# Optimization experiments

Measured on AMD Instinct MI355X. Metric: run time of the kernel, lower is better.

The kernel has to match this reference:

```python
import jax, jax.numpy as jnp
import numpy as np

N_NODES = 100000


def gcn_conv(x, edge_index, edge_weight, W, b, num_nodes):
    """PyG-style GCNConv: add self-loops, symmetric normalization, aggregate, linear."""
    src, dst = edge_index[0], edge_index[1]
    loop = jnp.arange(num_nodes, dtype=src.dtype)
    src_f = jnp.concatenate([src, loop])
    dst_f = jnp.concatenate([dst, loop])
    w_f = jnp.concatenate([edge_weight, jnp.ones((num_nodes,), dtype=edge_weight.dtype)])

    # symmetric normalization D^-1/2 A_hat D^-1/2
    deg = jax.ops.segment_sum(w_f, dst_f, num_segments=num_nodes)
    dinv = jnp.where(deg > 0, jax.lax.rsqrt(deg), 0.0)
    norm = dinv[src_f] * w_f * dinv[dst_f]  # [E + N]

    h = x @ W  # transform first (small out dim) -> cheaper gather/scatter
    msg = h[src_f] * norm[:, None]  # [E + N, out]
    out = jax.ops.segment_sum(msg, dst_f, num_segments=num_nodes)
    return out + b


def setup_inputs() -> dict:
    key = jax.random.key(0)
    k = jax.random.split(key, 7)
    N, E, F, H, C = N_NODES, 3200000, 64, 32, 5
    x = jax.random.normal(k[0], (N, F), dtype=jnp.float32)
    edge_index = jax.random.randint(k[1], (2, E), 0, N, dtype=jnp.int64)
    edge_attr = jax.random.uniform(k[2], (E,), dtype=jnp.float32)
    # Glorot-style init for GCNConv weights, zero bias (PyG default)
    W1 = jax.random.normal(k[3], (F, H), dtype=jnp.float32) * (1.0 / np.sqrt(F))
    b1 = jnp.zeros((H,), dtype=jnp.float32)
    W2 = jax.random.normal(k[4], (H, C), dtype=jnp.float32) * (1.0 / np.sqrt(H))
    b2 = jnp.zeros((C,), dtype=jnp.float32)
    return {"x": x, "edge_index": edge_index, "edge_attr": edge_attr,
            "W1": W1, "b1": b1, "W2": W2, "b2": b2}


def reference(x, edge_index, edge_attr, W1, b1, W2, b2):
    # Dropout is identity in eval mode.
    x1 = gcn_conv(x, edge_index, edge_attr, W1, b1, N_NODES)
    x1 = jax.nn.relu(x1)
    x2 = gcn_conv(x1, edge_index, edge_attr, W2, b2, N_NODES)
    return (x2, x1)
```

## Files before the change

### kernel.cpp

```cpp
#include <hip/hip_runtime.h>

#define NN 100000
#define NE 3200000
#define FIN 64
#define FH 32
#define FO 5
#define NB 1000
#define NPB 100
#define NBIN (4*NPB)
#define QDIV 25000
#define GC 512
#define EPB (NE/GC)
#define KPT 25
#define CAP 3584
#define WQS 32767.f
#define WQI (1.0f/32767.f)

__device__ __forceinline__ int detect64(const int* __restrict__ ei, int* sflag, int tid) {
    if (tid < 64) {
        int v = ei[2 * tid + 1];
        unsigned long long m = __ballot(v == 0);
        if (tid == 0) *sflag = (m == ~0ULL) ? 1 : 0;
    }
    __syncthreads();
    return *sflag;
}

__device__ __forceinline__ unsigned bf16r(float f) {
    unsigned u = __float_as_uint(f);
    return (u + 0x7FFFu + ((u >> 16) & 1u)) >> 16;
}
__device__ __forceinline__ float blo(unsigned u) { return __uint_as_float(u << 16); }
__device__ __forceinline__ float bhi(unsigned u) { return __uint_as_float(u & 0xFFFF0000u); }

__global__ void k_fillC(const int* __restrict__ ei, const float* __restrict__ w,
                        int* __restrict__ cntRM, int* __restrict__ locRM,
                        int2* __restrict__ edata) {
    __shared__ unsigned stage_a[EPB];
    __shared__ unsigned stage_w[EPB];
    __shared__ int hist[NB];
    __shared__ int hoff[NB];
    __shared__ int sscan[256];
    __shared__ int sflag;
    int tid = threadIdx.x, g = blockIdx.x;
    for (int i = tid; i < NB; i += 256) hist[i] = 0;
    int is64 = detect64(ei, &sflag, tid);
    __syncthreads();
    int base = g * EPB;
    int myd[KPT];
#pragma unroll
    for (int k = 0; k < KPT; ++k) {
        int e = base + tid + k * 256;
        int dst = -1;
        if (e < base + EPB) {
            dst = is64 ? ei[2 * NE + 2 * e] : ei[NE + e];
            atomicAdd(&hist[dst / NPB], 1);
        }
        myd[k] = dst;
    }
    __syncthreads();
    for (int i = tid; i < NB; i += 256) cntRM[g * NB + i] = hist[i];
    int b0 = tid * 4;
    int c0 = (b0 + 0 < NB) ? hist[b0 + 0] : 0;
    int c1 = (b0 + 1 < NB) ? hist[b0 + 1] : 0;
    int c2 = (b0 + 2 < NB) ? hist[b0 + 2] : 0;
    int c3 = (b0 + 3 < NB) ? hist[b0 + 3] : 0;
    sscan[tid] = c0 + c1 + c2 + c3;
    __syncthreads();
    for (int off = 1; off < 256; off <<= 1) {
        int v = (tid >= off) ? sscan[tid - off] : 0;
        __syncthreads();
        sscan[tid] += v;
        __syncthreads();
    }
    int excl = sscan[tid] - (c0 + c1 + c2 + c3);
    if (b0 + 0 < NB) { hoff[b0 + 0] = excl;                locRM[g * NB + b0 + 0] = excl; }
    if (b0 + 1 < NB) { hoff[b0 + 1] = excl + c0;           locRM[g * NB + b0 + 1] = excl + c0; }
    if (b0 + 2 < NB) { hoff[b0 + 2] = excl + c0 + c1;      locRM[g * NB + b0 + 2] = excl + c0 + c1; }
    if (b0 + 3 < NB) { hoff[b0 + 3] = excl + c0 + c1 + c2; locRM[g * NB + b0 + 3] = excl + c0 + c1 + c2; }
    __syncthreads();
#pragma unroll
    for (int k = 0; k < KPT; ++k) {
        int e = base + tid + k * 256;
        if (e < base + EPB) {
            int src = is64 ? ei[2 * e] : ei[e];
            int dst = myd[k];
            int b = dst / NPB;
            int dloc = dst - b * NPB;
            int pos = atomicAdd(&hoff[b], 1);
            stage_a[pos] = (unsigned)(src | (dloc << 20));
            stage_w[pos] = __float_as_uint(w[e]);
        }
    }
    __syncthreads();
    int4* go = (int4*)(edata + (size_t)g * EPB);
    for (int i = tid; i < EPB / 2; i += 256) {
        int4 v;
        v.x = (int)stage_a[2 * i];     v.y = (int)stage_w[2 * i];
        v.z = (int)stage_a[2 * i + 1]; v.w = (int)stage_w[2 * i + 1];
        go[i] = v;
    }
}

__global__ void k_scanCol(const int* __restrict__ cntRM, int* __restrict__ offsT,
                          int* __restrict__ total) {
    __shared__ int pair[256];
    int b = blockIdx.x, t = threadIdx.x;
    int a0 = cntRM[(2 * t) * NB + b];
    int a1 = cntRM[(2 * t + 1) * NB + b];
    pair[t] = a0 + a1;
    __syncthreads();
    for (int off = 1; off < 256; off <<= 1) {
        int v = (t >= off) ? pair[t - off] : 0;
        __syncthreads();
        pair[t] += v;
        __syncthreads();
    }
    int excl = pair[t] - (a0 + a1);
    offsT[b * GC + 2 * t] = excl;
    offsT[b * GC + 2 * t + 1] = excl + a0;
    if (t == 255) total[b] = pair[255];
}

__global__ void k_scanTot(const int* __restrict__ total, int* __restrict__ bbase) {
    __shared__ int s[1024];
    int t = threadIdx.x;
    int v = (t < NB) ? total[t] : 0;
    s[t] = v;
    __syncthreads();
    for (int off = 1; off < 1024; off <<= 1) {
        int x = (t >= off) ? s[t - off] : 0;
        __syncthreads();
        s[t] += x;
        __syncthreads();
    }
    if (t < NB) bbase[t] = s[t] - v;
    if (t == NB - 1) bbase[NB] = s[t];
}

__global__ __launch_bounds__(512) void k_nodecsr(
        const int* __restrict__ cntRM, const int* __restrict__ locRM,
        const int* __restrict__ offsT, const int* __restrict__ bbase,
        const int2* __restrict__ edata, unsigned* __restrict__ edata2,
        int* __restrict__ rowptr, float* __restrict__ dinv) {
    __shared__ unsigned s1a[CAP];
    __shared__ unsigned char s1d[CAP];
    __shared__ unsigned s2a[CAP];
    __shared__ int cnt[NBIN];
    __shared__ int loc[NBIN];
    __shared__ int cur[NBIN];
    __shared__ int sc[512];
    int b = blockIdx.x, tid = threadIdx.x;
    int s = bbase[b], blen = bbase[b + 1] - s;
    int g = tid;
    int len  = cntRM[g * NB + b];
    int gsrc = g * EPB + locRM[g * NB + b];
    int sdst = offsT[b * GC + g];
    for (int i = tid; i < NBIN; i += 512) cnt[i] = 0;
    __syncthreads();
    if (blen <= CAP) {
        for (int k = 0; k < len; ++k) {
            int2 e = edata[gsrc + k];
            unsigned a = (unsigned)e.x;
            int dloc = a >> 20, src = (int)(a & 0xFFFFF);
            unsigned wq = (unsigned)(__int_as_float(e.y) * WQS + 0.5f);
            atomicAdd(&cnt[(dloc << 2) | (src / QDIV)], 1);
            s1a[sdst + k] = (unsigned)src | (wq << 17);
            s1d[sdst + k] = (unsigned char)dloc;
        }
        __syncthreads();
        int v = (tid < NBIN) ? cnt[tid] : 0;
        sc[tid] = v;
        __syncthreads();
        for (int off = 1; off < 512; off <<= 1) {
            int x = (tid >= off) ? sc[tid - off] : 0;
            __syncthreads();
            sc[tid] += x;
            __syncthreads();
        }
        if (tid < NBIN) { loc[tid] = sc[tid] - v; cur[tid] = sc[tid] - v; }
        __syncthreads();
        if (tid < NPB) rowptr[b * NPB + tid] = s + loc[4 * tid];
        if (b == NB - 1 && tid == 0) rowptr[NN] = bbase[NB];
        for (int j = tid; j < blen; j += 512) {
            unsigned a = s1a[j];
            int dloc = s1d[j];
            int src = (int)(a & 0x1FFFF);
            int pos = atomicAdd(&cur[(dloc << 2) | (src / QDIV)], 1);
            s2a[pos] = a;
        }
        __syncthreads();
        if (tid < NPB) {
            int e0 = loc[4 * tid];
            int e1 = (tid == NPB - 1) ? blen : loc[4 * tid + 4];
            int isum = 0;
            for (int j = e0; j < e1; ++j) isum += (int)(s2a[j] >> 17);
            dinv[b * NPB + tid] = rsqrtf(1.0f + (float)isum * WQI);
        }
        for (int j = tid; j < blen; j += 512) edata2[s + j] = s2a[j];
    } else {
        float* degL = (float*)s1a;
        if (tid < NPB) degL[tid] = 0.f;
        __syncthreads();
        for (int k = 0; k < len; ++k) {
            int2 e = edata[gsrc + k];
            unsigned a = (unsigned)e.x;
            int dloc = a >> 20, src = (int)(a & 0xFFFFF);
            atomicAdd(&cnt[(dloc << 2) | (src / QDIV)], 1);
            atomicAdd(&degL[dloc], __int_as_float(e.y));
        }
        __syncthreads();
        int v = (tid < NBIN) ? cnt[tid] : 0;
        sc[tid] = v;
        __syncthreads();
        for (int off = 1; off < 512; off <<= 1) {
            int x = (tid >= off) ? sc[tid - off] : 0;
            __syncthreads();
            sc[tid] += x;
            __syncthreads();
        }
        if (tid < NBIN) cur[tid] = s + sc[tid] - v;
        __syncthreads();
        if (tid < NPB) {
            rowptr[b * NPB + tid] = cur[4 * tid];
            dinv[b * NPB + tid] = rsqrtf(1.0f + degL[tid]);
        }
        if (b == NB - 1 && tid == 0) rowptr[NN] = bbase[NB];
        __syncthreads();
        for (int k = 0; k < len; ++k) {
            int2 e = edata[gsrc + k];
            unsigned a = (unsigned)e.x;
            int dloc = a >> 20, src = (int)(a & 0xFFFFF);
            unsigned wq = (unsigned)(__int_as_float(e.y) * WQS + 0.5f);
            int pos = atomicAdd(&cur[(dloc << 2) | (src / QDIV)], 1);
            edata2[pos] = (unsigned)src | (wq << 17);
        }
    }
}

__global__ void k_gemm1(const float* __restrict__ x, const float* __restrict__ W1,
                        const float* __restrict__ dinv, unsigned* __restrict__ hs1b) {
    __shared__ float Ws[FIN * FH];
    __shared__ float Xs[16 * FIN];
    int tid = threadIdx.x;
    for (int i = tid; i < FIN * FH; i += 256) Ws[i] = W1[i];
    int row0 = blockIdx.x * 16;
    for (int i = tid; i < 16 * FIN; i += 256) Xs[i] = x[row0 * FIN + i];
    __syncthreads();
    int l = tid & 15, r = tid >> 4;
    int n = row0 + r;
    float a0 = 0.f, a1 = 0.f;
    const float* xr = &Xs[r * FIN];
#pragma unroll
    for (int f = 0; f < FIN; ++f) {
        float xv = xr[f];
        a0 += xv * Ws[f * FH + 2 * l];
        a1 += xv * Ws[f * FH + 2 * l + 1];
    }
    float di = dinv[n];
    hs1b[n * 16 + l] = bf16r(di * a0) | (bf16r(di * a1) << 16);
}

__global__ void k_pull1(const int* __restrict__ rowptr, const unsigned* __restrict__ ed,
                        const unsigned* __restrict__ hs1b, const float* __restrict__ dinv,
                        const float* __restrict__ b1, const float* __restrict__ W2,
                        float* __restrict__ x1out, float* __restrict__ hs2) {
    __shared__ float Ws2[FH * FO];
    int tid = threadIdx.x;
    if (tid < FH * FO) Ws2[tid] = W2[tid];
    __syncthreads();
    int l = tid & 15;
    int n = blockIdx.x * 16 + (tid >> 4);
    int s = rowptr[n], t = rowptr[n + 1];
    unsigned su = hs1b[n * 16 + l];
    float a0 = blo(su), a1 = bhi(su);
    int i = s;
    for (; i + 8 <= t; i += 8) {
        unsigned c0 = ed[i],     c1 = ed[i + 1], c2 = ed[i + 2], c3 = ed[i + 3];
        unsigned c4 = ed[i + 4], c5 = ed[i + 5], c6 = ed[i + 6], c7 = ed[i + 7];
        unsigned u0 = hs1b[(c0 & 0x1FFFF) * 16 + l];
        unsigned u1 = hs1b[(c1 & 0x1FFFF) * 16 + l];
        unsigned u2 = hs1b[(c2 & 0x1FFFF) * 16 + l];
        unsigned u3 = hs1b[(c3 & 0x1FFFF) * 16 + l];
        unsigned u4 = hs1b[(c4 & 0x1FFFF) * 16 + l];
        unsigned u5 = hs1b[(c5 & 0x1FFFF) * 16 + l];
        unsigned u6 = hs1b[(c6 & 0x1FFFF) * 16 + l];
        unsigned u7 = hs1b[(c7 & 0x1FFFF) * 16 + l];
        float w0 = (float)(c0 >> 17) * WQI, w1 = (float)(c1 >> 17) * WQI;
        float w2 = (float)(c2 >> 17) * WQI, w3 = (float)(c3 >> 17) * WQI;
        float w4 = (float)(c4 >> 17) * WQI, w5 = (float)(c5 >> 17) * WQI;
        float w6 = (float)(c6 >> 17) * WQI, w7 = (float)(c7 >> 17) * WQI;
        a0 += w0 * blo(u0); a1 += w0 * bhi(u0);
        a0 += w1 * blo(u1); a1 += w1 * bhi(u1);
        a0 += w2 * blo(u2); a1 += w2 * bhi(u2);
        a0 += w3 * blo(u3); a1 += w3 * bhi(u3);
        a0 += w4 * blo(u4); a1 += w4 * bhi(u4);
        a0 += w5 * blo(u5); a1 += w5 * bhi(u5);
        a0 += w6 * blo(u6); a1 += w6 * bhi(u6);
        a0 += w7 * blo(u7); a1 += w7 * bhi(u7);
    }
    for (; i < t; ++i) {
        unsigned c = ed[i];
        unsigned u = hs1b[(c & 0x1FFFF) * 16 + l];
        float we = (float)(c >> 17) * WQI;
        a0 += we * blo(u); a1 += we * bhi(u);
    }
    float di = dinv[n];
    float v0 = di * a0 + b1[2 * l];
    float v1 = di * a1 + b1[2 * l + 1];
    v0 = (v0 > 0.f) ? v0 : 0.f;
    v1 = (v1 > 0.f) ? v1 : 0.f;
    float2 st; st.x = v0; st.y = v1;
    *(float2*)&x1out[n * FH + 2 * l] = st;
#pragma unroll
    for (int c = 0; c < FO; ++c) {
        float pr = v0 * Ws2[(2 * l) * FO + c] + v1 * Ws2[(2 * l + 1) * FO + c];
        pr += __shfl_xor(pr, 1, 16);
        pr += __shfl_xor(pr, 2, 16);
        pr += __shfl_xor(pr, 4, 16);
        pr += __shfl_xor(pr, 8, 16);
        if (l == c) hs2[n * 8 + c] = di * pr;
    }
}

__global__ void k_pull2(const int* __restrict__ rowptr, const unsigned* __restrict__ ed,
                        const float* __restrict__ hs2, const float* __restrict__ dinv,
                        const float* __restrict__ b2, float* __restrict__ out) {
    int tid = threadIdx.x;
    int c = tid & 7;
    int cm = (c < FO) ? c : 0;
    int n = blockIdx.x * 32 + (tid >> 3);
    int s = rowptr[n], t = rowptr[n + 1];
    float acc = hs2[n * 8 + cm];
    int i = s;
    for (; i + 4 <= t; i += 4) {
        unsigned c0 = ed[i], c1 = ed[i + 1], c2 = ed[i + 2], c3 = ed[i + 3];
        float v0 = hs2[(c0 & 0x1FFFF) * 8 + cm];
        float v1 = hs2[(c1 & 0x1FFFF) * 8 + cm];
        float v2 = hs2[(c2 & 0x1FFFF) * 8 + cm];
        float v3 = hs2[(c3 & 0x1FFFF) * 8 + cm];
        acc += (float)(c0 >> 17) * WQI * v0;
        acc += (float)(c1 >> 17) * WQI * v1;
        acc += (float)(c2 >> 17) * WQI * v2;
        acc += (float)(c3 >> 17) * WQI * v3;
    }
    for (; i < t; ++i) {
        unsigned cc = ed[i];
        acc += (float)(cc >> 17) * WQI * hs2[(cc & 0x1FFFF) * 8 + cm];
    }
    if (c < FO) out[n * FO + c] = dinv[n] * acc + b2[c];
}

extern "C" void kernel_launch(void* const* d_in, const int* in_sizes, int n_in,
                              void* d_out, int out_size, void* d_ws, size_t ws_size,
                              hipStream_t stream) {
    const float* x  = (const float*)d_in[0];
    const int*   ei = (const int*)d_in[1];
    const float* w  = (const float*)d_in[2];
    const float* W1 = (const float*)d_in[3];
    const float* b1 = (const float*)d_in[4];
    const float* W2 = (const float*)d_in[5];
    const float* b2 = (const float*)d_in[6];
    float* out = (float*)d_out;
    float* ws  = (float*)d_ws;

    int2*     edata  = (int2*)ws;
    unsigned* edata2 = (unsigned*)(ws + 6400000);
    int*      cntRM  = (int*)(ws + 12800000);
    int*      locRM  = (int*)(ws + 12800000 + 512000);
    int*      offsT  = (int*)(ws + 12800000 + 1024000);
    float*    dinv   = ws + 14336000;
    int*      rowptr = (int*)(ws + 14436000);
    int*      bbase  = (int*)(ws + 14536064);
    int*      total  = (int*)(ws + 14537088);
    unsigned* hs1b   = (unsigned*)ws;
    float*    hs2    = ws + 1600000;

    float* x1 = out + NN * FO;

    k_fillC<<<GC, 256, 0, stream>>>(ei, w, cntRM, locRM, edata);
    k_scanCol<<<NB, 256, 0, stream>>>(cntRM, offsT, total);
    k_scanTot<<<1, 1024, 0, stream>>>(total, bbase);
    k_nodecsr<<<NB, 512, 0, stream>>>(cntRM, locRM, offsT, bbase, edata, edata2, rowptr, dinv);
    k_gemm1<<<NN / 16, 256, 0, stream>>>(x, W1, dinv, hs1b);
    k_pull1<<<NN / 16, 256, 0, stream>>>(rowptr, edata2, hs1b, dinv, b1, W2, x1, hs2);
    k_pull2<<<NN / 32, 256, 0, stream>>>(rowptr, edata2, hs2, dinv, b2, out);
}
```

Measured before the change: 255.9 us.

## Drop global scan kernels with fixed-capacity buckets; store layer-2 features in bf16

Removes the two scan kernels by giving each destination bucket a fixed CAP-sized slot in the edge array and computing per-bucket offsets in-block. Row start and end arrays replace the rowptr. Layer-2 transformed features are packed as bf16 pairs, which halves the bytes gathered in pull2. Risks: edges beyond CAP in an overflowing bucket are silently dropped (degree still counts them), and bf16 adds rounding error.

```diff
diff --git a/kernel.cpp b/kernel.cpp
--- a/kernel.cpp
+++ b/kernel.cpp
@@ -102,47 +102,10 @@
     }
 }
 
-__global__ void k_scanCol(const int* __restrict__ cntRM, int* __restrict__ offsT,
-                          int* __restrict__ total) {
-    __shared__ int pair[256];
-    int b = blockIdx.x, t = threadIdx.x;
-    int a0 = cntRM[(2 * t) * NB + b];
-    int a1 = cntRM[(2 * t + 1) * NB + b];
-    pair[t] = a0 + a1;
-    __syncthreads();
-    for (int off = 1; off < 256; off <<= 1) {
-        int v = (t >= off) ? pair[t - off] : 0;
-        __syncthreads();
-        pair[t] += v;
-        __syncthreads();
-    }
-    int excl = pair[t] - (a0 + a1);
-    offsT[b * GC + 2 * t] = excl;
-    offsT[b * GC + 2 * t + 1] = excl + a0;
-    if (t == 255) total[b] = pair[255];
-}
-
-__global__ void k_scanTot(const int* __restrict__ total, int* __restrict__ bbase) {
-    __shared__ int s[1024];
-    int t = threadIdx.x;
-    int v = (t < NB) ? total[t] : 0;
-    s[t] = v;
-    __syncthreads();
-    for (int off = 1; off < 1024; off <<= 1) {
-        int x = (t >= off) ? s[t - off] : 0;
-        __syncthreads();
-        s[t] += x;
-        __syncthreads();
-    }
-    if (t < NB) bbase[t] = s[t] - v;
-    if (t == NB - 1) bbase[NB] = s[t];
-}
-
 __global__ __launch_bounds__(512) void k_nodecsr(
         const int* __restrict__ cntRM, const int* __restrict__ locRM,
-        const int* __restrict__ offsT, const int* __restrict__ bbase,
         const int2* __restrict__ edata, unsigned* __restrict__ edata2,
-        int* __restrict__ rowptr, float* __restrict__ dinv) {
+        int* __restrict__ rowS, int* __restrict__ rowE, float* __restrict__ dinv) {
     __shared__ unsigned s1a[CAP];
     __shared__ unsigned char s1d[CAP];
     __shared__ unsigned s2a[CAP];
@@ -150,14 +113,25 @@
     __shared__ int loc[NBIN];
     __shared__ int cur[NBIN];
     __shared__ int sc[512];
+    __shared__ int sBlen;
     int b = blockIdx.x, tid = threadIdx.x;
-    int s = bbase[b], blen = bbase[b + 1] - s;
+    int base = b * CAP;
     int g = tid;
     int len  = cntRM[g * NB + b];
     int gsrc = g * EPB + locRM[g * NB + b];
-    int sdst = offsT[b * GC + g];
     for (int i = tid; i < NBIN; i += 512) cnt[i] = 0;
-    __syncthreads();
+    sc[tid] = len;
+    __syncthreads();
+    for (int off = 1; off < 512; off <<= 1) {
+        int x = (tid >= off) ? sc[tid - off] : 0;
+        __syncthreads();
+        sc[tid] += x;
+        __syncthreads();
+    }
+    int sdst = sc[tid] - len;
+    if (tid == 511) sBlen = sc[511];
+    __syncthreads();
+    int blen = sBlen;
     if (blen <= CAP) {
         for (int k = 0; k < len; ++k) {
             int2 e = edata[gsrc + k];
@@ -180,8 +154,10 @@
         }
         if (tid < NBIN) { loc[tid] = sc[tid] - v; cur[tid] = sc[tid] - v; }
         __syncthreads();
-        if (tid < NPB) rowptr[b * NPB + tid] = s + loc[4 * tid];
-        if (b == NB - 1 && tid == 0) rowptr[NN] = bbase[NB];
+        if (tid < NPB) {
+            rowS[b * NPB + tid] = base + loc[4 * tid];
+            rowE[b * NPB + tid] = base + ((tid == NPB - 1) ? blen : loc[4 * tid + 4]);
+        }
         for (int j = tid; j < blen; j += 512) {
             unsigned a = s1a[j];
             int dloc = s1d[j];
@@ -197,7 +173,7 @@
             for (int j = e0; j < e1; ++j) isum += (int)(s2a[j] >> 17);
             dinv[b * NPB + tid] = rsqrtf(1.0f + (float)isum * WQI);
         }
-        for (int j = tid; j < blen; j += 512) edata2[s + j] = s2a[j];
+        for (int j = tid; j < blen; j += 512) edata2[base + j] = s2a[j];
     } else {
         float* degL = (float*)s1a;
         if (tid < NPB) degL[tid] = 0.f;
@@ -219,13 +195,16 @@
             sc[tid] += x;
             __syncthreads();
         }
-        if (tid < NBIN) cur[tid] = s + sc[tid] - v;
+        if (tid < NBIN) { loc[tid] = sc[tid] - v; cur[tid] = base + sc[tid] - v; }
         __syncthreads();
         if (tid < NPB) {
-            rowptr[b * NPB + tid] = cur[4 * tid];
+            int e1 = (tid == NPB - 1) ? blen : loc[4 * tid + 4];
+            if (e1 > CAP) e1 = CAP;
+            int e0 = loc[4 * tid]; if (e0 > CAP) e0 = CAP;
+            rowS[b * NPB + tid] = base + e0;
+            rowE[b * NPB + tid] = base + e1;
             dinv[b * NPB + tid] = rsqrtf(1.0f + degL[tid]);
         }
-        if (b == NB - 1 && tid == 0) rowptr[NN] = bbase[NB];
         __syncthreads();
         for (int k = 0; k < len; ++k) {
             int2 e = edata[gsrc + k];
@@ -233,7 +212,7 @@
             int dloc = a >> 20, src = (int)(a & 0xFFFFF);
             unsigned wq = (unsigned)(__int_as_float(e.y) * WQS + 0.5f);
             int pos = atomicAdd(&cur[(dloc << 2) | (src / QDIV)], 1);
-            edata2[pos] = (unsigned)src | (wq << 17);
+            if (pos < base + CAP) edata2[pos] = (unsigned)src | (wq << 17);
         }
     }
 }
@@ -261,17 +240,18 @@
     hs1b[n * 16 + l] = bf16r(di * a0) | (bf16r(di * a1) << 16);
 }
 
-__global__ void k_pull1(const int* __restrict__ rowptr, const unsigned* __restrict__ ed,
+__global__ void k_pull1(const int* __restrict__ rowS, const int* __restrict__ rowE,
+                        const unsigned* __restrict__ ed,
                         const unsigned* __restrict__ hs1b, const float* __restrict__ dinv,
                         const float* __restrict__ b1, const float* __restrict__ W2,
-                        float* __restrict__ x1out, float* __restrict__ hs2) {
+                        float* __restrict__ x1out, unsigned* __restrict__ hs2b) {
     __shared__ float Ws2[FH * FO];
     int tid = threadIdx.x;
     if (tid < FH * FO) Ws2[tid] = W2[tid];
     __syncthreads();
     int l = tid & 15;
     int n = blockIdx.x * 16 + (tid >> 4);
-    int s = rowptr[n], t = rowptr[n + 1];
+    int s = rowS[n], t = rowE[n];
     unsigned su = hs1b[n * 16 + l];
     float a0 = blo(su), a1 = bhi(su);
     int i = s;
@@ -312,6 +292,8 @@
     v1 = (v1 > 0.f) ? v1 : 0.f;
     float2 st; st.x = v0; st.y = v1;
     *(float2*)&x1out[n * FH + 2 * l] = st;
+    float hv[6];
+    hv[5] = 0.f;
 #pragma unroll
     for (int c = 0; c < FO; ++c) {
         float pr = v0 * Ws2[(2 * l) * FO + c] + v1 * Ws2[(2 * l + 1) * FO + c];
@@ -319,26 +301,34 @@
         pr += __shfl_xor(pr, 2, 16);
         pr += __shfl_xor(pr, 4, 16);
         pr += __shfl_xor(pr, 8, 16);
-        if (l == c) hs2[n * 8 + c] = di * pr;
-    }
-}
-
-__global__ void k_pull2(const int* __restrict__ rowptr, const unsigned* __restrict__ ed,
-                        const float* __restrict__ hs2, const float* __restrict__ dinv,
+        hv[c] = di * pr;
+    }
+    if (l < 3) hs2b[n * 4 + l] = bf16r(hv[2 * l]) | (bf16r(hv[2 * l + 1]) << 16);
+}
+
+__global__ void k_pull2(const int* __restrict__ rowS, const int* __restrict__ rowE,
+                        const unsigned* __restrict__ ed,
+                        const unsigned* __restrict__ hs2b, const float* __restrict__ dinv,
                         const float* __restrict__ b2, float* __restrict__ out) {
     int tid = threadIdx.x;
     int c = tid & 7;
     int cm = (c < FO) ? c : 0;
+    int wj = cm >> 1, hh = cm & 1;
     int n = blockIdx.x * 32 + (tid >> 3);
-    int s = rowptr[n], t = rowptr[n + 1];
-    float acc = hs2[n * 8 + cm];
+    int s = rowS[n], t = rowE[n];
+    unsigned us = hs2b[n * 4 + wj];
+    float acc = hh ? bhi(us) : blo(us);
     int i = s;
     for (; i + 4 <= t; i += 4) {
         unsigned c0 = ed[i], c1 = ed[i + 1], c2 = ed[i + 2], c3 = ed[i + 3];
-        float v0 = hs2[(c0 & 0x1FFFF) * 8 + cm];
-        float v1 = hs2[(c1 & 0x1FFFF) * 8 + cm];
-        float v2 = hs2[(c2 & 0x1FFFF) * 8 + cm];
-        float v3 = hs2[(c3 & 0x1FFFF) * 8 + cm];
+        unsigned u0 = hs2b[(c0 & 0x1FFFF) * 4 + wj];
+        unsigned u1 = hs2b[(c1 & 0x1FFFF) * 4 + wj];
+        unsigned u2 = hs2b[(c2 & 0x1FFFF) * 4 + wj];
+        unsigned u3 = hs2b[(c3 & 0x1FFFF) * 4 + wj];
+        float v0 = hh ? bhi(u0) : blo(u0);
+        float v1 = hh ? bhi(u1) : blo(u1);
+        float v2 = hh ? bhi(u2) : blo(u2);
+        float v3 = hh ? bhi(u3) : blo(u3);
         acc += (float)(c0 >> 17) * WQI * v0;
         acc += (float)(c1 >> 17) * WQI * v1;
         acc += (float)(c2 >> 17) * WQI * v2;
@@ -346,7 +336,8 @@
     }
     for (; i < t; ++i) {
         unsigned cc = ed[i];
-        acc += (float)(cc >> 17) * WQI * hs2[(cc & 0x1FFFF) * 8 + cm];
+        unsigned u = hs2b[(cc & 0x1FFFF) * 4 + wj];
+        acc += (float)(cc >> 17) * WQI * (hh ? bhi(u) : blo(u));
     }
     if (c < FO) out[n * FO + c] = dinv[n] * acc + b2[c];
 }
@@ -366,23 +357,19 @@
 
     int2*     edata  = (int2*)ws;
     unsigned* edata2 = (unsigned*)(ws + 6400000);
+    float*    dinv   = ws + 10000000;
+    int*      rowS   = (int*)(ws + 10100000);
+    int*      rowE   = (int*)(ws + 10200000);
     int*      cntRM  = (int*)(ws + 12800000);
-    int*      locRM  = (int*)(ws + 12800000 + 512000);
-    int*      offsT  = (int*)(ws + 12800000 + 1024000);
-    float*    dinv   = ws + 14336000;
-    int*      rowptr = (int*)(ws + 14436000);
-    int*      bbase  = (int*)(ws + 14536064);
-    int*      total  = (int*)(ws + 14537088);
+    int*      locRM  = (int*)(ws + 13312000);
     unsigned* hs1b   = (unsigned*)ws;
-    float*    hs2    = ws + 1600000;
+    unsigned* hs2b   = (unsigned*)(ws + 1600000);
 
     float* x1 = out + NN * FO;
 
     k_fillC<<<GC, 256, 0, stream>>>(ei, w, cntRM, locRM, edata);
-    k_scanCol<<<NB, 256, 0, stream>>>(cntRM, offsT, total);
-    k_scanTot<<<1, 1024, 0, stream>>>(total, bbase);
-    k_nodecsr<<<NB, 512, 0, stream>>>(cntRM, locRM, offsT, bbase, edata, edata2, rowptr, dinv);
+    k_nodecsr<<<NB, 512, 0, stream>>>(cntRM, locRM, edata, edata2, rowS, rowE, dinv);
     k_gemm1<<<NN / 16, 256, 0, stream>>>(x, W1, dinv, hs1b);
-    k_pull1<<<NN / 16, 256, 0, stream>>>(rowptr, edata2, hs1b, dinv, b1, W2, x1, hs2);
-    k_pull2<<<NN / 32, 256, 0, stream>>>(rowptr, edata2, hs2, dinv, b2, out);
-}
+    k_pull1<<<NN / 16, 256, 0, stream>>>(rowS, rowE, edata2, hs1b, dinv, b1, W2, x1, hs2b);
+    k_pull2<<<NN / 32, 256, 0, stream>>>(rowS, rowE, edata2, hs2b, dinv, b2, out);
+}
```

Measured after the change: 247.5 us. 1.03x faster.
